# Optimization experiments

Hardware: AMD Instinct MI355X
Metric: run time of the kernel (lower is better)

## Reference

```python
import jax, jax.numpy as jnp
import numpy as np

B_SZ, SEQ, D_MODEL = 2, 4096, 2048
EXPAND, D_STATE, D_CONV = 2, 16, 4
D_INNER = EXPAND * D_MODEL          # 4096
DT_RANK = -(-D_MODEL // 16)         # 128


def setup_inputs() -> dict:
    key = jax.random.key(0)
    ks = jax.random.split(key, 9)
    s = 0.02
    hidden_states = jax.random.normal(ks[0], (B_SZ, SEQ, D_MODEL), jnp.float32)
    W_in = jax.random.normal(ks[1], (2 * D_INNER, D_MODEL), jnp.float32) * s
    conv_w = jax.random.normal(ks[2], (D_INNER, D_CONV), jnp.float32) * 0.2
    conv_b = jnp.zeros((D_INNER,), jnp.float32)
    W_x = jax.random.normal(ks[3], (DT_RANK + 2 * D_STATE, D_INNER), jnp.float32) * s
    W_dt = jax.random.normal(ks[4], (D_INNER, DT_RANK), jnp.float32) * (DT_RANK ** -0.5)
    # dt bias so softplus(dt) ~ [1e-3, 0.1] as in Mamba init
    u = jax.random.uniform(ks[5], (D_INNER,), jnp.float32)
    dt = jnp.exp(u * (np.log(0.1) - np.log(1e-3)) + np.log(1e-3))
    dt_bias = dt + jnp.log(-jnp.expm1(-dt))  # inverse softplus
    # S4D-real init: A = -[1..d_state] per channel (kept negative for stability)
    A = -jnp.tile(jnp.arange(1.0, D_STATE + 1.0, dtype=jnp.float32), (D_INNER, 1))
    D = jnp.ones((D_INNER,), jnp.float32)
    W_out = jax.random.normal(ks[6], (D_MODEL, D_INNER), jnp.float32) * s
    return {"hidden_states": hidden_states, "W_in": W_in, "conv_w": conv_w,
            "conv_b": conv_b, "W_x": W_x, "W_dt": W_dt, "dt_bias": dt_bias,
            "A": A, "D": D, "W_out": W_out}


def _mamba_fwd(hidden_states, W_in, conv_w, conv_b, W_x, W_dt, dt_bias, A, D, W_out):
    # in_proj -> (B, L, 2*d_inner); split into x and gate z
    xz = jnp.einsum('bld,ed->ble', hidden_states, W_in)
    x, z = jnp.split(xz, 2, axis=-1)                    # (B,L,d_inner) each
    # causal depthwise conv1d over L (kernel d_conv), then SiLU
    d_conv = conv_w.shape[1]
    xp = jnp.pad(x, ((0, 0), (d_conv - 1, 0), (0, 0)))
    L = x.shape[1]
    xc = conv_b
    acc = jnp.zeros_like(x)
    for k in range(d_conv):                             # small fixed loop (4 taps)
        acc = acc + xp[:, k:k + L, :] * conv_w[:, k]
    x = jax.nn.silu(acc + conv_b)
    # x_proj -> dt_rank + 2*d_state
    ssm = jnp.einsum('bld,ed->ble', x, W_x)
    dt_r, Bm, Cm = jnp.split(ssm, [DT_RANK, DT_RANK + D_STATE], axis=-1)
    delta = jax.nn.softplus(jnp.einsum('blr,dr->bld', dt_r, W_dt) + dt_bias)
    # selective scan: h_t = exp(delta_t*A) h_{t-1} + delta_t*B_t*u_t ; y_t = C_t.h_t
    def step(state, inp):
        d_t, u_t, B_t, C_t = inp                        # (B,Di),(B,Di),(B,N),(B,N)
        dA = jnp.exp(d_t[..., None] * A)                # (B,Di,N)
        state = state * dA + (d_t * u_t)[..., None] * B_t[:, None, :]
        y = jnp.einsum('bdn,bn->bd', state, C_t)
        return state, y
    init = jnp.zeros((x.shape[0], D_INNER, D_STATE), jnp.float32)
    xs = (jnp.swapaxes(delta, 0, 1), jnp.swapaxes(x, 0, 1),
          jnp.swapaxes(Bm, 0, 1), jnp.swapaxes(Cm, 0, 1))
    _, ys = jax.lax.scan(step, init, xs)
    y = jnp.swapaxes(ys, 0, 1) + x * D                  # D skip connection
    y = y * jax.nn.silu(z)                              # gate
    return jnp.einsum('bld,md->blm', y, W_out)


def reference(hidden_states, W_in, conv_w, conv_b, W_x, W_dt, dt_bias, A, D, W_out):
    return _mamba_fwd(hidden_states, W_in, conv_w, conv_b, W_x, W_dt,
                      dt_bias, A, D, W_out)
```

## Files before the change

kernel.cpp:

```cpp
#include <hip/hip_runtime.h>
#include <hip/hip_bf16.h>
#include <cstdint>
#include <cstddef>

typedef _Float16 f16x8 __attribute__((ext_vector_type(8)));
typedef _Float16 f16x4 __attribute__((ext_vector_type(4)));
typedef float    f32x4 __attribute__((ext_vector_type(4)));

#define AS1 __attribute__((address_space(1)))
#define AS3 __attribute__((address_space(3)))

static constexpr int B_SZ = 2, SEQ = 4096, D_MODEL = 2048;
static constexpr int D_INNER = 4096, D_STATE = 16, D_CONV = 4, DT_RANK = 128;
static constexpr int M_ROWS = B_SZ * SEQ;
static constexpr int SSM_W  = DT_RANK + 2 * D_STATE;
static constexpr int KSPLIT = 8, KSLICE = 512;

__global__ __launch_bounds__(256) void k_cvt_all(
    const float* __restrict__ s0, const float* __restrict__ s1,
    const float* __restrict__ s2, const float* __restrict__ s3,
    const float* __restrict__ s4,
    _Float16* __restrict__ d0, _Float16* __restrict__ d1,
    _Float16* __restrict__ d2, _Float16* __restrict__ d3,
    _Float16* __restrict__ d4) {
    const int i = blockIdx.x * 256 + threadIdx.x;
    const float* s; _Float16* d; int off;
    if (i < 4194304)      { s = s0; d = d0; off = i; }
    else if (i < 8388608) { s = s1; d = d1; off = i - 4194304; }
    else if (i < 8552448) { s = s2; d = d2; off = i - 8388608; }
    else if (i < 8683520) { s = s3; d = d3; off = i - 8552448; }
    else                  { s = s4; d = d4; off = i - 8683520; }
    f32x4 v = ((const f32x4*)s)[off];
    f16x4 h;
    h[0] = (_Float16)v[0]; h[1] = (_Float16)v[1];
    h[2] = (_Float16)v[2]; h[3] = (_Float16)v[3];
    ((f16x4*)d)[off] = h;
}

template <int EPI>
__global__ __launch_bounds__(512, 2) void k_gemm256p(
    const _Float16* __restrict__ A, const _Float16* __restrict__ Bm, int K, int nby,
    void* __restrict__ out0, void* __restrict__ out1, int ldc) {
    __shared__ _Float16 lA[2][256][64];
    __shared__ _Float16 lB[2][256][64];
    constexpr int LBUF  = 32768;
    constexpr int LBUFH = 16384;

    const int tid = threadIdx.x, l = tid & 63, w = tid >> 6;
    const int fr = l & 15, fq = l >> 4;
    const int wrA = (w >> 2) * 128;
    const int wcB = (w & 3) * 64;

    const int nwg = gridDim.x, qq = nwg >> 3;
    const int id = (blockIdx.x & 7) * qq + (blockIdx.x >> 3);
    const int by = id % nby, bx = id / nby;
    const int tileM = by * 256, tileN = bx * 256;

    const int rsub = l >> 3;
    const int gco  = ((l & 7) ^ rsub) << 3;
    const int swz0 = (fq ^ (fr & 7)) << 4;

    const char* cA = (const char*)lA;
    const char* cB = (const char*)lB;
    const int bA0 = (wrA + fr) * 128 + swz0;
    const int bA1 = bA0 ^ 64;
    const int bB0 = (wcB + fr) * 128 + swz0;
    const int bB1 = bB0 ^ 64;

    const _Float16* pA[4];
    const _Float16* pB[4];
    _Float16* dA[4];
    _Float16* dB[4];
#pragma unroll
    for (int u = 0; u < 4; ++u) {
        const int brow = (u >> 1) * 128 + (w * 2 + (u & 1)) * 8;
        pA[u] = A  + (size_t)(tileM + brow + rsub) * K + gco;
        pB[u] = Bm + (size_t)(tileN + brow + rsub) * K + gco;
        dA[u] = &lA[0][brow][0];
        dB[u] = &lB[0][brow][0];
    }

    const int NK = K >> 6;

    f32x4 acc[8][4];
#pragma unroll
    for (int m = 0; m < 8; m++)
#pragma unroll
        for (int n = 0; n < 4; n++) acc[m][n] = (f32x4)0.f;

#pragma unroll
    for (int t = 0; t < 2; ++t) {
#pragma unroll
        for (int u = 0; u < 4; ++u)
            __builtin_amdgcn_global_load_lds((const AS1 void*)(pA[u] + t * 64),
                (AS3 void*)(dA[u] + t * LBUFH), 16, 0, 0);
#pragma unroll
        for (int u = 0; u < 4; ++u)
            __builtin_amdgcn_global_load_lds((const AS1 void*)(pB[u] + t * 64),
                (AS3 void*)(dB[u] + t * LBUFH), 16, 0, 0);
    }
#pragma unroll
    for (int u = 0; u < 4; ++u) { pA[u] += 128; pB[u] += 128; }
    asm volatile("s_waitcnt vmcnt(8)" ::: "memory");
    __builtin_amdgcn_s_barrier();

    f16x8 af[4][2], bf0[2][2], bf1[2][2];

#define MFMA_QUAD(MO, NO, BF)                                                        \
    __builtin_amdgcn_s_setprio(1);                                                   \
    _Pragma("unroll") for (int m = 0; m < 4; ++m)                                    \
    _Pragma("unroll") for (int n = 0; n < 2; ++n)                                    \
    _Pragma("unroll") for (int kk = 0; kk < 2; ++kk)                                 \
        acc[(MO) + m][(NO) + n] = __builtin_amdgcn_mfma_f32_16x16x32_f16(            \
            af[m][kk], BF[n][kk], acc[(MO) + m][(NO) + n], 0, 0, 0);                 \
    __builtin_amdgcn_s_setprio(0);

#define KTILE(BUF, KOFF, PF, DOEND)                                                  \
          \
    _Pragma("unroll")                                                                \
    for (int m = 0; m < 4; ++m) {                                                    \
        af[m][0] = *(const f16x8*)(cA + (BUF) * LBUF + bA0 + m * 2048);              \
        af[m][1] = *(const f16x8*)(cA + (BUF) * LBUF + bA1 + m * 2048);              \
    }                                                                                \
    _Pragma("unroll")                                                                \
    for (int n = 0; n < 2; ++n) {                                                    \
        bf0[n][0] = *(const f16x8*)(cB + (BUF) * LBUF + bB0 + n * 2048);             \
        bf0[n][1] = *(const f16x8*)(cB + (BUF) * LBUF + bB1 + n * 2048);             \
    }                                                                                \
    _Pragma("unroll")                                                                \
    for (int n = 0; n < 2; ++n) {                                                    \
        bf1[n][0] = *(const f16x8*)(cB + (BUF) * LBUF + bB0 + (n + 2) * 2048);       \
        bf1[n][1] = *(const f16x8*)(cB + (BUF) * LBUF + bB1 + (n + 2) * 2048);       \
    }                                                                                \
    asm volatile("s_waitcnt lgkmcnt(4)" ::: "memory");     \
    __builtin_amdgcn_sched_barrier(0);                                               \
    MFMA_QUAD(0, 0, bf0)                                                             \
    asm volatile("s_waitcnt lgkmcnt(0)" ::: "memory");                 \
    __builtin_amdgcn_sched_barrier(0);                                               \
    MFMA_QUAD(0, 2, bf1)                                                             \
    __builtin_amdgcn_s_barrier();                \
    _Pragma("unroll")                                                                \
    for (int m = 0; m < 4; ++m) {                                                    \
        af[m][0] = *(const f16x8*)(cA + (BUF) * LBUF + bA0 + (m + 4) * 2048);        \
        af[m][1] = *(const f16x8*)(cA + (BUF) * LBUF + bA1 + (m + 4) * 2048);        \
    }                                                                                \
    if (PF) {                                                                        \
        _Pragma("unroll")                                                            \
        for (int u = 0; u < 4; ++u)                                                  \
            __builtin_amdgcn_global_load_lds((const AS1 void*)(pB[u] + (KOFF)),      \
                (AS3 void*)(dB[u] + (BUF) * LBUFH), 16, 0, 0);                       \
    }                                                                                \
    asm volatile("s_waitcnt lgkmcnt(0)" ::: "memory");               \
    __builtin_amdgcn_sched_barrier(0);                                               \
    MFMA_QUAD(4, 0, bf0)                                                             \
    __builtin_amdgcn_s_barrier();               \
    if (PF) {                                                                        \
        _Pragma("unroll")                                                            \
        for (int u = 0; u < 4; ++u)                                                  \
            __builtin_amdgcn_global_load_lds((const AS1 void*)(pA[u] + (KOFF)),      \
                (AS3 void*)(dA[u] + (BUF) * LBUFH), 16, 0, 0);                       \
    }                                                                                \
    MFMA_QUAD(4, 2, bf1)                                                             \
    if (DOEND) {                                                                     \
        if (PF) { asm volatile("s_waitcnt vmcnt(8)" ::: "memory"); }                 \
        else    { asm volatile("s_waitcnt vmcnt(0)" ::: "memory"); }                 \
        __builtin_amdgcn_s_barrier();                 \
    }

    for (int kt = 0; kt < NK; kt += 2) {
        const bool pf0 = (kt + 2 < NK);
        const bool pf1 = (kt + 3 < NK);
        KTILE(0, 0, pf0, true)
        KTILE(1, 64, pf1, pf0)
#pragma unroll
        for (int u = 0; u < 4; ++u) { pA[u] += 128; pB[u] += 128; }
    }
#undef KTILE
#undef MFMA_QUAD

#pragma unroll
    for (int m = 0; m < 8; ++m) {
#pragma unroll
        for (int n = 0; n < 4; ++n) {
            const int r0 = tileM + wrA + m * 16 + fq * 4;
            const int c  = tileN + wcB + n * 16 + fr;
#pragma unroll
            for (int q = 0; q < 4; ++q) {
                const float  v  = acc[m][n][q];
                const size_t mm = (size_t)(r0 + q);
                if (EPI == 0) {
                    if (c < D_INNER)
                        ((_Float16*)out0)[mm * D_INNER + c] = (_Float16)v;
                    else
                        ((_Float16*)out1)[mm * D_INNER + (c - D_INNER)] = (_Float16)v;
                } else {
                    ((float*)out0)[mm * ldc + c] = v;
                }
            }
        }
    }
}

template <int BM, int BN, int EPI>
__global__ __launch_bounds__(256) void k_gemm_nt(
    const _Float16* __restrict__ A, const _Float16* __restrict__ Bm, int K,
    int lda, int ldb, void* __restrict__ out0, void* __restrict__ out1,
    const float* __restrict__ bias, int ldc) {
    __shared__ _Float16 a_lds[BM][32];
    __shared__ _Float16 b_lds[BN][32];
    constexpr int MR = BM / 32;
    constexpr int NR = BN / 32;
    const int tid  = threadIdx.x;
    const int lane = tid & 63;
    const int wid  = tid >> 6;
    const int wr = wid >> 1, wc = wid & 1;
    const int tileM = blockIdx.y * BM;
    const int tileN = blockIdx.x * BN;
    const int kz = (EPI == 4) ? blockIdx.z * KSLICE : 0;

    f32x4 acc[MR][NR];
    for (int i = 0; i < MR; i++)
        for (int j = 0; j < NR; j++) acc[i][j] = (f32x4)0.f;

    constexpr int IS_A = BM / 16;
    constexpr int IS_B = BN / 16;
    const int srow = lane >> 2;
    const int skof = (lane & 3) * 8;
    const int fr = lane & 15, fq = lane >> 4;

    for (int kk = 0; kk < K; kk += 32) {
        if (kk) __syncthreads();
        for (int is = wid; is < IS_A + IS_B; is += 4) {
            const bool isA = is < IS_A;
            const int  li  = isA ? is : is - IS_A;
            const int  row = li * 16 + srow;
            const _Float16* g =
                isA ? (A  + (size_t)(tileM + row) * lda + kz + kk + skof)
                    : (Bm + (size_t)(tileN + row) * ldb + kz + kk + skof);
            char* lp = ((char*)(isA ? &a_lds[0][0] : &b_lds[0][0])) + (size_t)li * 1024;
            __builtin_amdgcn_global_load_lds((const AS1 void*)g, (AS3 void*)lp, 16, 0, 0);
        }
        __syncthreads();

        f16x8 af[MR], bf[NR];
#pragma unroll
        for (int i = 0; i < MR; i++)
            af[i] = *(const f16x8*)&a_lds[wr * (BM / 2) + i * 16 + fr][fq * 8];
#pragma unroll
        for (int j = 0; j < NR; j++)
            bf[j] = *(const f16x8*)&b_lds[wc * (BN / 2) + j * 16 + fr][fq * 8];
#pragma unroll
        for (int i = 0; i < MR; i++)
#pragma unroll
            for (int j = 0; j < NR; j++)
                acc[i][j] = __builtin_amdgcn_mfma_f32_16x16x32_f16(af[i], bf[j], acc[i][j], 0, 0, 0);
    }

#pragma unroll
    for (int i = 0; i < MR; i++) {
#pragma unroll
        for (int j = 0; j < NR; j++) {
            const int r0 = tileM + wr * (BM / 2) + i * 16 + fq * 4;
            const int c  = tileN + wc * (BN / 2) + j * 16 + fr;
#pragma unroll
            for (int q = 0; q < 4; q++) {
                const float  v = acc[i][j][q];
                const size_t m = (size_t)(r0 + q);
                if (EPI == 1) {
                    ((float*)out0)[m * ldc + c] = v;
                } else if (EPI == 2) {
                    float x  = v + bias[c];
                    float sp = (x > 20.f) ? x : log1pf(__expf(x));
                    ((_Float16*)out0)[m * ldc + c] = (_Float16)sp;
                } else if (EPI == 3) {
                    ((float*)out0)[m * ldc + c] = v;
                    if (c < DT_RANK)
                        ((_Float16*)out1)[m * DT_RANK + c] = (_Float16)v;
                } else {
                    ((float*)out0)[(size_t)blockIdx.z * M_ROWS * SSM_W + m * ldc + c] = v;
                }
            }
        }
    }
}

__global__ __launch_bounds__(256) void k_xred(const float* __restrict__ pbuf,
                                              float* __restrict__ ssm,
                                              _Float16* __restrict__ dtr) {
    const int i = blockIdx.x * 256 + threadIdx.x;
    const int m = i / SSM_W;
    const int c = i - m * SSM_W;
    float s = 0.f;
#pragma unroll
    for (int z = 0; z < KSPLIT; ++z)
        s += pbuf[(size_t)z * M_ROWS * SSM_W + i];
    ssm[i] = s;
    if (c < DT_RANK) dtr[(size_t)m * DT_RANK + c] = (_Float16)s;
}

__global__ __launch_bounds__(256) void k_conv_silu(const _Float16* __restrict__ x,
                                                   const float* __restrict__ w,
                                                   const float* __restrict__ bias,
                                                   _Float16* __restrict__ out) {
    const int idx = blockIdx.x * 256 + threadIdx.x;
    const int d4 = idx & (D_INNER / 4 - 1);
    const int t  = (idx >> 10) & (SEQ - 1);
    const int b  = idx >> 22;
    const int d  = d4 * 4;
    const size_t rowbase = (size_t)b * SEQ * D_INNER;

    f32x4 wv[4];
#pragma unroll
    for (int i = 0; i < 4; i++) wv[i] = ((const f32x4*)w)[d + i];

    float acc[4];
#pragma unroll
    for (int i = 0; i < 4; i++) acc[i] = bias[d + i];
#pragma unroll
    for (int k = 0; k < D_CONV; k++) {
        int ti = t - (D_CONV - 1) + k;
        if (ti < 0) continue;
        f16x4 xv = *(const f16x4*)&x[rowbase + (size_t)ti * D_INNER + d];
#pragma unroll
        for (int i = 0; i < 4; i++) acc[i] += (float)xv[i] * wv[i][k];
    }
    f16x4 o;
#pragma unroll
    for (int i = 0; i < 4; i++) {
        float v = acc[i];
        o[i] = (_Float16)(v / (1.f + __expf(-v)));
    }
    *(f16x4*)&out[rowbase + (size_t)t * D_INNER + d] = o;
}

template <int CH, typename ST>
__global__ __launch_bounds__(256) void k_scan_p1(const _Float16* __restrict__ delta_h,
                                                 const _Float16* __restrict__ xc,
                                                 const float* __restrict__ ssm,
                                                 const float* __restrict__ Aptr,
                                                 ST* __restrict__ Sbuf,
                                                 ST* __restrict__ Pbuf) {
    constexpr int NCH = SEQ / CH;
    constexpr float L2E = 1.44269504088896f;
    const int bid   = blockIdx.x;
    const int dg    = bid & 15;
    const int chunk = (bid >> 4) % NCH;
    const int b     = bid / (16 * NCH);
    const int d     = dg * 256 + threadIdx.x;

    __shared__ float bsh[CH][D_STATE];
    const size_t rb = (size_t)b * SEQ + (size_t)chunk * CH;
    for (int i = threadIdx.x; i < CH * D_STATE; i += 256) {
        int t = i >> 4, n = i & 15;
        bsh[t][n] = ssm[(rb + t) * SSM_W + DT_RANK + n];
    }
    __syncthreads();

    float a2[D_STATE];
#pragma unroll
    for (int n = 0; n < D_STATE; n++) a2[n] = Aptr[(size_t)d * D_STATE + n] * L2E;
    float st[D_STATE];
#pragma unroll
    for (int n = 0; n < D_STATE; n++) st[n] = 0.f;
    float dtsum = 0.f;

    for (int t = 0; t < CH; t += 4) {
        const size_t i0 = (rb + t) * D_INNER + d;
        float dtv[4], uv[4];
#pragma unroll
        for (int j = 0; j < 4; ++j) {
            dtv[j] = (float)delta_h[i0 + (size_t)j * D_INNER];
            uv[j]  = (float)xc[i0 + (size_t)j * D_INNER];
        }
#pragma unroll
        for (int j = 0; j < 4; ++j) {
            const float du = dtv[j] * uv[j];
            dtsum += dtv[j];
#pragma unroll
            for (int n = 0; n < D_STATE; n++) {
                float p = exp2f(dtv[j] * a2[n]);
                st[n] = st[n] * p + du * bsh[t + j][n];
            }
        }
    }
    const size_t ob = ((size_t)(b * NCH + chunk) * D_STATE) * D_INNER + d;
#pragma unroll
    for (int n = 0; n < D_STATE; n++) {
        Sbuf[ob + (size_t)n * D_INNER] = (ST)st[n];
        Pbuf[ob + (size_t)n * D_INNER] = (ST)exp2f(dtsum * a2[n]);
    }
}

template <int NCH, typename ST>
__global__ __launch_bounds__(256) void k_scan_p2(ST* __restrict__ Sbuf,
                                                 const ST* __restrict__ Pbuf) {
    const int id = blockIdx.x * 256 + threadIdx.x;
    const int d = id & (D_INNER - 1);
    const int n = (id >> 12) & 15;
    const int b = id >> 16;
    float h = 0.f;
    for (int c = 0; c < NCH; ++c) {
        const size_t off = ((size_t)((b * NCH + c) * D_STATE + n)) * D_INNER + d;
        const float Pv = (float)Pbuf[off];
        const float Sv = (float)Sbuf[off];
        Sbuf[off] = (ST)h;
        h = Pv * h + Sv;
    }
}

template <int CH, typename ST>
__global__ __launch_bounds__(256) void k_scan_p3(const _Float16* __restrict__ delta_h,
                                                 const _Float16* __restrict__ xc,
                                                 const float* __restrict__ ssm,
                                                 const _Float16* __restrict__ z,
                                                 const float* __restrict__ Aptr,
                                                 const float* __restrict__ Dptr,
                                                 const ST* __restrict__ Sbuf,
                                                 _Float16* __restrict__ y_out) {
    constexpr int NCH = SEQ / CH;
    constexpr float L2E = 1.44269504088896f;
    const int bid   = blockIdx.x;
    const int dg    = bid & 15;
    const int chunk = (bid >> 4) % NCH;
    const int b     = bid / (16 * NCH);
    const int d     = dg * 256 + threadIdx.x;

    __shared__ float bsh[CH][2 * D_STATE];
    const size_t rb = (size_t)b * SEQ + (size_t)chunk * CH;
    for (int i = threadIdx.x; i < CH * 2 * D_STATE; i += 256) {
        int t = i >> 5, j = i & 31;
        bsh[t][j] = ssm[(rb + t) * SSM_W + DT_RANK + j];
    }
    __syncthreads();

    float a2[D_STATE];
#pragma unroll
    for (int n = 0; n < D_STATE; n++) a2[n] = Aptr[(size_t)d * D_STATE + n] * L2E;
    const float Dd = Dptr[d];

    const size_t ob = ((size_t)(b * NCH + chunk) * D_STATE) * D_INNER + d;
    float st[D_STATE];
#pragma unroll
    for (int n = 0; n < D_STATE; n++) st[n] = (float)Sbuf[ob + (size_t)n * D_INNER];

    for (int t = 0; t < CH; t += 4) {
        const size_t i0 = (rb + t) * D_INNER + d;
        float dtv[4], uv[4], zv[4];
#pragma unroll
        for (int j = 0; j < 4; ++j) {
            dtv[j] = (float)delta_h[i0 + (size_t)j * D_INNER];
            uv[j]  = (float)xc[i0 + (size_t)j * D_INNER];
            zv[j]  = (float)z[i0 + (size_t)j * D_INNER];
        }
#pragma unroll
        for (int j = 0; j < 4; ++j) {
            const float du = dtv[j] * uv[j];
            float y = 0.f;
#pragma unroll
            for (int n = 0; n < D_STATE; n++) {
                float p = exp2f(dtv[j] * a2[n]);
                st[n] = st[n] * p + du * bsh[t + j][n];
                y += st[n] * bsh[t + j][D_STATE + n];
            }
            const float g = zv[j] / (1.f + __expf(-zv[j]));
            y_out[i0 + (size_t)j * D_INNER] = (_Float16)((y + uv[j] * Dd) * g);
        }
    }
}

__global__ __launch_bounds__(256) void k_scan(const _Float16* __restrict__ delta_h,
                                              const _Float16* __restrict__ xc,
                                              const float* __restrict__ ssm,
                                              const _Float16* __restrict__ z,
                                              const float* __restrict__ Aptr,
                                              const float* __restrict__ Dptr,
                                              _Float16* __restrict__ y_out) {
    const int b = blockIdx.x >> 4;
    const int d = (blockIdx.x & 15) * 256 + threadIdx.x;
    constexpr float L2E = 1.44269504088896f;
    float a2[D_STATE];
#pragma unroll
    for (int n = 0; n < D_STATE; n++) a2[n] = Aptr[(size_t)d * D_STATE + n] * L2E;
    const float Dd = Dptr[d];
    float st[D_STATE];
#pragma unroll
    for (int n = 0; n < D_STATE; n++) st[n] = 0.f;
    __shared__ float bc[128][32];
    const size_t rb = (size_t)b * SEQ;
    for (int tc = 0; tc < SEQ; tc += 128) {
        __syncthreads();
        for (int i = threadIdx.x; i < 128 * 32; i += 256) {
            int tl = i >> 5, j = i & 31;
            bc[tl][j] = ssm[(rb + tc + tl) * SSM_W + DT_RANK + j];
        }
        __syncthreads();
        for (int tl = 0; tl < 128; ++tl) {
            const size_t idx = (rb + tc + tl) * D_INNER + d;
            const float dt = (float)delta_h[idx];
            const float u  = (float)xc[idx];
            const float du = dt * u;
            float y = 0.f;
#pragma unroll
            for (int n = 0; n < D_STATE; n++) {
                float dA = exp2f(dt * a2[n]);
                st[n] = st[n] * dA + du * bc[tl][n];
                y += st[n] * bc[tl][D_STATE + n];
            }
            const float zv = (float)z[idx];
            const float g  = zv / (1.f + __expf(-zv));
            y_out[idx] = (_Float16)((y + u * Dd) * g);
        }
    }
}

template <int CH, typename ST>
static void launch_chunked_scan(const _Float16* delta_h, const _Float16* xc,
                                const float* ssm, const _Float16* z,
                                const float* Aptr, const float* Dptr,
                                ST* S, ST* P, _Float16* y, hipStream_t stream) {
    constexpr int NCH = SEQ / CH;
    k_scan_p1<CH, ST><<<B_SZ * NCH * 16, 256, 0, stream>>>(delta_h, xc, ssm, Aptr, S, P);
    k_scan_p2<NCH, ST><<<(B_SZ * 16 * D_INNER) / 256, 256, 0, stream>>>(S, P);
    k_scan_p3<CH, ST><<<B_SZ * NCH * 16, 256, 0, stream>>>(delta_h, xc, ssm, z, Aptr, Dptr, S, y);
}

extern "C" void kernel_launch(void* const* d_in, const int* in_sizes, int n_in,
                              void* d_out, int out_size, void* d_ws, size_t ws_size,
                              hipStream_t stream) {
    const float* hs    = (const float*)d_in[0];
    const float* W_in  = (const float*)d_in[1];
    const float* convw = (const float*)d_in[2];
    const float* convb = (const float*)d_in[3];
    const float* W_x   = (const float*)d_in[4];
    const float* W_dt  = (const float*)d_in[5];
    const float* dtb   = (const float*)d_in[6];
    const float* Aptr  = (const float*)d_in[7];
    const float* Dptr  = (const float*)d_in[8];
    const float* W_out = (const float*)d_in[9];

    char* ws = (char*)d_ws;
    _Float16* hs_h    = (_Float16*)(ws + 0);
    _Float16* Win_h   = (_Float16*)(ws + 33554432);
    _Float16* y_h     = (_Float16*)(ws + 0);
    _Float16* xraw    = (_Float16*)(ws + 67108864);
    float*    pbuf    = (float*)   (ws + 67108864);
    _Float16* delta_h = (_Float16*)(ws + 67108864);
    _Float16* xc      = (_Float16*)(ws + 134217728);
    float*    ssm     = (float*)   (ws + 201326592);
    _Float16* dtr     = (_Float16*)(ws + 206569472);
    _Float16* Wx_h    = (_Float16*)(ws + 208666624);
    _Float16* Wdt_h   = (_Float16*)(ws + 209977344);
    _Float16* Wout_h  = (_Float16*)(ws + 211025920);
    _Float16* z_h     = (_Float16*)d_out;
    const size_t spbase = 227803136ull;

    k_cvt_all<<<42112, 256, 0, stream>>>(hs, W_in, W_x, W_dt, W_out,
                                         hs_h, Win_h, Wx_h, Wdt_h, Wout_h);

    k_gemm256p<0><<<(M_ROWS / 256) * (2 * D_INNER / 256), 512, 0, stream>>>(
        hs_h, Win_h, D_MODEL, M_ROWS / 256, xraw, z_h, 0);

    k_conv_silu<<<(B_SZ * SEQ * (D_INNER / 4)) / 256, 256, 0, stream>>>(xraw, convw, convb, xc);

    k_gemm_nt<64, 32, 4><<<dim3(SSM_W / 32, M_ROWS / 64, KSPLIT), 256, 0, stream>>>(
        xc, Wx_h, KSLICE, D_INNER, D_INNER, pbuf, nullptr, nullptr, SSM_W);
    k_xred<<<(M_ROWS * SSM_W) / 256, 256, 0, stream>>>(pbuf, ssm, dtr);

    k_gemm_nt<128, 128, 2><<<dim3(D_INNER / 128, M_ROWS / 128), 256, 0, stream>>>(
        dtr, Wdt_h, DT_RANK, DT_RANK, DT_RANK, delta_h, nullptr, dtb, D_INNER);

    {
        const size_t e64  = (size_t)B_SZ * (SEQ / 64)  * D_STATE * D_INNER;
        const size_t e128 = (size_t)B_SZ * (SEQ / 128) * D_STATE * D_INNER;
        if (ws_size >= spbase + 2 * e64 * sizeof(float)) {
            float* S = (float*)(ws + spbase);
            float* P = S + e64;
            launch_chunked_scan<64, float>(delta_h, xc, ssm, z_h, Aptr, Dptr, S, P, y_h, stream);
        } else if (ws_size >= spbase + 2 * e128 * sizeof(float)) {
            float* S = (float*)(ws + spbase);
            float* P = S + e128;
            launch_chunked_scan<128, float>(delta_h, xc, ssm, z_h, Aptr, Dptr, S, P, y_h, stream);
        } else if (ws_size >= spbase + 2 * e128 * sizeof(_Float16)) {
            _Float16* S = (_Float16*)(ws + spbase);
            _Float16* P = S + e128;
            launch_chunked_scan<128, _Float16>(delta_h, xc, ssm, z_h, Aptr, Dptr, S, P, y_h, stream);
        } else {
            k_scan<<<B_SZ * (D_INNER / 256), 256, 0, stream>>>(delta_h, xc, ssm, z_h, Aptr, Dptr, y_h);
        }
    }

    k_gemm256p<1><<<(M_ROWS / 256) * (D_MODEL / 256), 512, 0, stream>>>(
        y_h, Wout_h, D_INNER, M_ROWS / 256, d_out, nullptr, D_MODEL);
}
```

Measured before the change: 1.099 ms.

## Widen fp16 conversion, drop split-K x_proj, store scan chunk states in fp16

The weight/activation conversion kernel now handles eight floats per thread with 16-byte stores and half the blocks. The x_proj GEMM drops the 8-way split-K and its separate reduction kernel, running the full K=4096 in one pass with the EPI 3 epilogue writing ssm and dtr directly. The chunked scan now always prefers 64-length chunks with fp16 inter-chunk state buffers instead of fp32. These changes cut memory traffic and one launch, but the x_proj GEMM launches far fewer blocks (about 640) with a long K loop, and fp16 chunk states lose precision.

```diff
diff --git a/kernel.cpp b/kernel.cpp
--- a/kernel.cpp
+++ b/kernel.cpp
@@ -14,7 +14,6 @@
 static constexpr int D_INNER = 4096, D_STATE = 16, D_CONV = 4, DT_RANK = 128;
 static constexpr int M_ROWS = B_SZ * SEQ;
 static constexpr int SSM_W  = DT_RANK + 2 * D_STATE;
-static constexpr int KSPLIT = 8, KSLICE = 512;
 
 __global__ __launch_bounds__(256) void k_cvt_all(
     const float* __restrict__ s0, const float* __restrict__ s1,
@@ -25,16 +24,19 @@
     _Float16* __restrict__ d4) {
     const int i = blockIdx.x * 256 + threadIdx.x;
     const float* s; _Float16* d; int off;
-    if (i < 4194304)      { s = s0; d = d0; off = i; }
-    else if (i < 8388608) { s = s1; d = d1; off = i - 4194304; }
-    else if (i < 8552448) { s = s2; d = d2; off = i - 8388608; }
-    else if (i < 8683520) { s = s3; d = d3; off = i - 8552448; }
-    else                  { s = s4; d = d4; off = i - 8683520; }
-    f32x4 v = ((const f32x4*)s)[off];
-    f16x4 h;
-    h[0] = (_Float16)v[0]; h[1] = (_Float16)v[1];
-    h[2] = (_Float16)v[2]; h[3] = (_Float16)v[3];
-    ((f16x4*)d)[off] = h;
+    if (i < 2097152)      { s = s0; d = d0; off = i; }
+    else if (i < 4194304) { s = s1; d = d1; off = i - 2097152; }
+    else if (i < 4276224) { s = s2; d = d2; off = i - 4194304; }
+    else if (i < 4341760) { s = s3; d = d3; off = i - 4276224; }
+    else                  { s = s4; d = d4; off = i - 4341760; }
+    f32x4 v0 = ((const f32x4*)s)[off * 2];
+    f32x4 v1 = ((const f32x4*)s)[off * 2 + 1];
+    f16x8 h;
+    h[0] = (_Float16)v0[0]; h[1] = (_Float16)v0[1];
+    h[2] = (_Float16)v0[2]; h[3] = (_Float16)v0[3];
+    h[4] = (_Float16)v1[0]; h[5] = (_Float16)v1[1];
+    h[6] = (_Float16)v1[2]; h[7] = (_Float16)v1[3];
+    ((f16x8*)d)[off] = h;
 }
 
 template <int EPI>
@@ -216,7 +218,6 @@
     const int wr = wid >> 1, wc = wid & 1;
     const int tileM = blockIdx.y * BM;
     const int tileN = blockIdx.x * BN;
-    const int kz = (EPI == 4) ? blockIdx.z * KSLICE : 0;
 
     f32x4 acc[MR][NR];
     for (int i = 0; i < MR; i++)
@@ -235,8 +236,8 @@
             const int  li  = isA ? is : is - IS_A;
             const int  row = li * 16 + srow;
             const _Float16* g =
-                isA ? (A  + (size_t)(tileM + row) * lda + kz + kk + skof)
-                    : (Bm + (size_t)(tileN + row) * ldb + kz + kk + skof);
+                isA ? (A  + (size_t)(tileM + row) * lda + kk + skof)
+                    : (Bm + (size_t)(tileN + row) * ldb + kk + skof);
             char* lp = ((char*)(isA ? &a_lds[0][0] : &b_lds[0][0])) + (size_t)li * 1024;
             __builtin_amdgcn_global_load_lds((const AS1 void*)g, (AS3 void*)lp, 16, 0, 0);
         }
@@ -272,30 +273,14 @@
                     float x  = v + bias[c];
                     float sp = (x > 20.f) ? x : log1pf(__expf(x));
                     ((_Float16*)out0)[m * ldc + c] = (_Float16)sp;
-                } else if (EPI == 3) {
+                } else {
                     ((float*)out0)[m * ldc + c] = v;
                     if (c < DT_RANK)
                         ((_Float16*)out1)[m * DT_RANK + c] = (_Float16)v;
-                } else {
-                    ((float*)out0)[(size_t)blockIdx.z * M_ROWS * SSM_W + m * ldc + c] = v;
                 }
             }
         }
     }
-}
-
-__global__ __launch_bounds__(256) void k_xred(const float* __restrict__ pbuf,
-                                              float* __restrict__ ssm,
-                                              _Float16* __restrict__ dtr) {
-    const int i = blockIdx.x * 256 + threadIdx.x;
-    const int m = i / SSM_W;
-    const int c = i - m * SSM_W;
-    float s = 0.f;
-#pragma unroll
-    for (int z = 0; z < KSPLIT; ++z)
-        s += pbuf[(size_t)z * M_ROWS * SSM_W + i];
-    ssm[i] = s;
-    if (c < DT_RANK) dtr[(size_t)m * DT_RANK + c] = (_Float16)s;
 }
 
 __global__ __launch_bounds__(256) void k_conv_silu(const _Float16* __restrict__ x,
@@ -543,7 +528,6 @@
     _Float16* Win_h   = (_Float16*)(ws + 33554432);
     _Float16* y_h     = (_Float16*)(ws + 0);
     _Float16* xraw    = (_Float16*)(ws + 67108864);
-    float*    pbuf    = (float*)   (ws + 67108864);
     _Float16* delta_h = (_Float16*)(ws + 67108864);
     _Float16* xc      = (_Float16*)(ws + 134217728);
     float*    ssm     = (float*)   (ws + 201326592);
@@ -554,7 +538,7 @@
     _Float16* z_h     = (_Float16*)d_out;
     const size_t spbase = 227803136ull;
 
-    k_cvt_all<<<42112, 256, 0, stream>>>(hs, W_in, W_x, W_dt, W_out,
+    k_cvt_all<<<21056, 256, 0, stream>>>(hs, W_in, W_x, W_dt, W_out,
                                          hs_h, Win_h, Wx_h, Wdt_h, Wout_h);
 
     k_gemm256p<0><<<(M_ROWS / 256) * (2 * D_INNER / 256), 512, 0, stream>>>(
@@ -562,9 +546,8 @@
 
     k_conv_silu<<<(B_SZ * SEQ * (D_INNER / 4)) / 256, 256, 0, stream>>>(xraw, convw, convb, xc);
 
-    k_gemm_nt<64, 32, 4><<<dim3(SSM_W / 32, M_ROWS / 64, KSPLIT), 256, 0, stream>>>(
-        xc, Wx_h, KSLICE, D_INNER, D_INNER, pbuf, nullptr, nullptr, SSM_W);
-    k_xred<<<(M_ROWS * SSM_W) / 256, 256, 0, stream>>>(pbuf, ssm, dtr);
+    k_gemm_nt<64, 32, 3><<<dim3(SSM_W / 32, M_ROWS / 64), 256, 0, stream>>>(
+        xc, Wx_h, D_INNER, D_INNER, D_INNER, ssm, dtr, nullptr, SSM_W);
 
     k_gemm_nt<128, 128, 2><<<dim3(D_INNER / 128, M_ROWS / 128), 256, 0, stream>>>(
         dtr, Wdt_h, DT_RANK, DT_RANK, DT_RANK, delta_h, nullptr, dtb, D_INNER);
@@ -572,14 +555,10 @@
     {
         const size_t e64  = (size_t)B_SZ * (SEQ / 64)  * D_STATE * D_INNER;
         const size_t e128 = (size_t)B_SZ * (SEQ / 128) * D_STATE * D_INNER;
-        if (ws_size >= spbase + 2 * e64 * sizeof(float)) {
-            float* S = (float*)(ws + spbase);
-            float* P = S + e64;
-            launch_chunked_scan<64, float>(delta_h, xc, ssm, z_h, Aptr, Dptr, S, P, y_h, stream);
-        } else if (ws_size >= spbase + 2 * e128 * sizeof(float)) {
-            float* S = (float*)(ws + spbase);
-            float* P = S + e128;
-            launch_chunked_scan<128, float>(delta_h, xc, ssm, z_h, Aptr, Dptr, S, P, y_h, stream);
+        if (ws_size >= spbase + 2 * e64 * sizeof(_Float16)) {
+            _Float16* S = (_Float16*)(ws + spbase);
+            _Float16* P = S + e64;
+            launch_chunked_scan<64, _Float16>(delta_h, xc, ssm, z_h, Aptr, Dptr, S, P, y_h, stream);
         } else if (ws_size >= spbase + 2 * e128 * sizeof(_Float16)) {
             _Float16* S = (_Float16*)(ws + spbase);
             _Float16* P = S + e128;
```

Result: faster. 1.060 ms (-3.6%).
